# Performance work log

Hardware: AMD Instinct MI355X
Metric: run time of the kernel (lower is better)

The kernel has to match this reference:

```python
import jax, jax.numpy as jnp
import numpy as np

B, T, U = 2048, 200, 128


def setup_inputs() -> dict:
    key = jax.random.key(0)
    ks = jax.random.split(key, 9)
    s = 1.0 / np.sqrt(U)
    inp = {
        "interest_states": jax.random.normal(ks[0], (B, T, U), dtype=jnp.float32),
        "attention_scores": jax.random.uniform(ks[1], (B, T, 1), dtype=jnp.float32),
        "W_xu": jax.random.normal(ks[2], (U, U), dtype=jnp.float32) * s,
        "b_xu": jnp.zeros((U,), dtype=jnp.float32),
        "W_hu": jax.random.normal(ks[3], (U, U), dtype=jnp.float32) * s,
        "b_hu": jnp.zeros((U,), dtype=jnp.float32),
        "W_xr": jax.random.normal(ks[4], (U, U), dtype=jnp.float32) * s,
        "b_xr": jnp.zeros((U,), dtype=jnp.float32),
        "W_hr": jax.random.normal(ks[5], (U, U), dtype=jnp.float32) * s,
        "b_hr": jnp.zeros((U,), dtype=jnp.float32),
        "W_xc": jax.random.normal(ks[6], (U, U), dtype=jnp.float32) * s,
        "b_xc": jnp.zeros((U,), dtype=jnp.float32),
        "W_hc": jax.random.normal(ks[7], (U, U), dtype=jnp.float32) * s,
        "b_hc": jnp.zeros((U,), dtype=jnp.float32),
    }
    return inp


def reference(interest_states, attention_scores, W_xu, b_xu, W_hu, b_hu,
              W_xr, b_xr, W_hr, b_hr, W_xc, b_xc, W_hc, b_hc):
    # Precompute input-side projections for all timesteps (batched GEMMs).
    xu = jnp.einsum('btu,uv->btv', interest_states, W_xu) + b_xu  # [B,T,U]
    xr = jnp.einsum('btu,uv->btv', interest_states, W_xr) + b_xr
    xc = jnp.einsum('btu,uv->btv', interest_states, W_xc) + b_xc
    # Time-major for scan: [T,B,U] / [T,B,1]
    xu_t = jnp.swapaxes(xu, 0, 1)
    xr_t = jnp.swapaxes(xr, 0, 1)
    xc_t = jnp.swapaxes(xc, 0, 1)
    att_t = jnp.swapaxes(attention_scores, 0, 1)  # [T,B,1]

    def step(h, inp):
        xu_i, xr_i, xc_i, a_i = inp
        u = jax.nn.sigmoid(xu_i + h @ W_hu + b_hu)       # update gate [B,U]
        r = jax.nn.sigmoid(xr_i + h @ W_hr + b_hr)       # reset gate  [B,U]
        c = jnp.tanh(xc_i + (r * h) @ W_hc + b_hc)       # candidate   [B,U]
        au = a_i * u                                     # attention-scaled update gate
        h_new = (1.0 - au) * h + au * c
        return h_new, None

    h0 = jnp.zeros((interest_states.shape[0], W_hu.shape[0]), dtype=interest_states.dtype)
    h_final, _ = jax.lax.scan(step, h0, (xu_t, xr_t, xc_t, att_t))
    return h_final  # [B,U]
```

## Files before the change

### kernel.cpp

```cpp
#include <hip/hip_runtime.h>
#include <hip/hip_bf16.h>

#define B_  2048
#define T_  200
#define U_  128
#define NB  8
#define PITCH 136

typedef __attribute__((ext_vector_type(8))) short short8;
typedef __attribute__((ext_vector_type(2))) short short2_t;
typedef __attribute__((ext_vector_type(4))) float f32x4;
typedef __attribute__((ext_vector_type(2))) float f32x2;

static __device__ inline short f2bf(float f) {
  union { float f; unsigned u; } v; v.f = f;
  unsigned r = v.u + 0x7FFFu + ((v.u >> 16) & 1u);
  return (short)(r >> 16);
}
static __device__ inline float sigm(float x) {
  return __builtin_amdgcn_rcpf(1.0f + __builtin_amdgcn_exp2f(x * -1.44269504088896340736f));
}
static __device__ inline float tanh_fast(float x) {
  return 1.0f - 2.0f * __builtin_amdgcn_rcpf(1.0f + __builtin_amdgcn_exp2f(x * 2.88539008177792681472f));
}

__global__ void prep_weights(const float* __restrict__ Wxu, const float* __restrict__ Wxr,
                             const float* __restrict__ Wxc, const float* __restrict__ Whu,
                             const float* __restrict__ Whr, const float* __restrict__ Whc,
                             short* __restrict__ out) {
  const int m = blockIdx.x >> 7;
  const int k = blockIdx.x & 127;
  const int n = threadIdx.x;
  const float* Wp;
  switch (m) {
    case 0: Wp = Wxu; break; case 1: Wp = Wxr; break; case 2: Wp = Wxc; break;
    case 3: Wp = Whu; break; case 4: Wp = Whr; break; default: Wp = Whc; break;
  }
  out[(m * 128 + n) * 128 + k] = f2bf(Wp[k * 128 + n]);
}

__global__ __launch_bounds__(512, 2) void augru_scan(
    const float* __restrict__ IS, const float* __restrict__ ATT,
    const float* __restrict__ bxu, const float* __restrict__ bhu,
    const float* __restrict__ bxr, const float* __restrict__ bhr,
    const float* __restrict__ bxc, const float* __restrict__ bhc,
    const short* __restrict__ WT, float* __restrict__ out) {
  __shared__ short h_bf[16][PITCH];
  __shared__ short x_bf[16][PITCH];
  __shared__ short rh_bf[16][PITCH];
  __shared__ float att_s[T_][NB];

  const int tid  = threadIdx.x;
  const int w    = tid >> 6;
  const int l    = tid & 63;
  const int l15  = l & 15;
  const int lg   = l >> 4;
  const int b0   = blockIdx.x * NB;
  const int colb = w * 16;
  const int col  = colb + l15;

  for (int i = tid; i < 16 * PITCH / 2; i += 512) {
    ((int*)h_bf)[i] = 0; ((int*)x_bf)[i] = 0; ((int*)rh_bf)[i] = 0;
  }
  for (int i = tid; i < T_ * NB; i += 512) {
    int r = i / T_, t = i % T_;
    att_s[t][r] = ATT[(size_t)(b0 + r) * T_ + t];
  }
  const int prow = w;
  const int pc2  = (tid & 63) * 2;
  {
    f32x2 xv = *(const f32x2*)(IS + ((size_t)(b0 + prow) * T_ + 0) * U_ + pc2);
    short2_t xb; xb[0] = f2bf(xv[0]); xb[1] = f2bf(xv[1]);
    *(short2_t*)&x_bf[prow][pc2] = xb;
  }
  short8 Wf[6][4];
#pragma unroll
  for (int m = 0; m < 6; ++m)
#pragma unroll
    for (int kf = 0; kf < 4; ++kf)
      Wf[m][kf] = *(const short8*)(WT + ((m * 128 + col) * 128 + kf * 32 + lg * 8));
  const float bu = bxu[col] + bhu[col];
  const float br = bxr[col] + bhr[col];
  const float bc = bxc[col] + bhc[col];

  const f32x4 fz = {0.0f, 0.0f, 0.0f, 0.0f};
  f32x4 hreg = fz;
  float ureg[4];

  for (int t = 0; t < T_; ++t) {
    __syncthreads();
    short8 xa[4], ha[4];
#pragma unroll
    for (int kf = 0; kf < 4; ++kf) {
      xa[kf] = *(const short8*)&x_bf[l15][kf * 32 + lg * 8];
      ha[kf] = *(const short8*)&h_bf[l15][kf * 32 + lg * 8];
    }
    const int tn = (t < T_ - 1) ? t + 1 : t;
    f32x2 xnext = *(const f32x2*)(IS + ((size_t)(b0 + prow) * T_ + tn) * U_ + pc2);

    f32x4 axu = fz, axr = fz, axc = fz, ahu = fz, ahr = fz;
#pragma unroll
    for (int kf = 0; kf < 4; ++kf) {
      axu = __builtin_amdgcn_mfma_f32_16x16x32_bf16(xa[kf], Wf[0][kf], axu, 0, 0, 0);
      axr = __builtin_amdgcn_mfma_f32_16x16x32_bf16(xa[kf], Wf[1][kf], axr, 0, 0, 0);
      axc = __builtin_amdgcn_mfma_f32_16x16x32_bf16(xa[kf], Wf[2][kf], axc, 0, 0, 0);
      ahu = __builtin_amdgcn_mfma_f32_16x16x32_bf16(ha[kf], Wf[3][kf], ahu, 0, 0, 0);
      ahr = __builtin_amdgcn_mfma_f32_16x16x32_bf16(ha[kf], Wf[4][kf], ahr, 0, 0, 0);
    }
#pragma unroll
    for (int rg = 0; rg < 4; ++rg) {
      float ug = sigm(axu[rg] + ahu[rg] + bu);
      float rr = sigm(axr[rg] + ahr[rg] + br);
      ureg[rg] = ug;
      rh_bf[lg * 4 + rg][col] = f2bf(rr * hreg[rg]);
    }
    __syncthreads();
    short8 ra[4];
#pragma unroll
    for (int kf = 0; kf < 4; ++kf) ra[kf] = *(const short8*)&rh_bf[l15][kf * 32 + lg * 8];
    f32x4 ahc = fz;
#pragma unroll
    for (int kf = 0; kf < 4; ++kf)
      ahc = __builtin_amdgcn_mfma_f32_16x16x32_bf16(ra[kf], Wf[5][kf], ahc, 0, 0, 0);
    f32x4 a4 = *(const f32x4*)&att_s[t][(lg & 1) * 4];
#pragma unroll
    for (int rg = 0; rg < 4; ++rg) {
      float cc = tanh_fast(axc[rg] + ahc[rg] + bc);
      float au = a4[rg] * ureg[rg];
      float hv = (1.0f - au) * hreg[rg] + au * cc;
      hreg[rg] = hv;
      h_bf[lg * 4 + rg][col] = f2bf(hv);
    }
    {
      short2_t xb; xb[0] = f2bf(xnext[0]); xb[1] = f2bf(xnext[1]);
      *(short2_t*)&x_bf[prow][pc2] = xb;
    }
  }
#pragma unroll
  for (int rg = 0; rg < 4; ++rg) {
    const int row = lg * 4 + rg;
    if (row < NB) out[(size_t)(b0 + row) * U_ + col] = hreg[rg];
  }
}

extern "C" void kernel_launch(void* const* d_in, const int* in_sizes, int n_in,
                              void* d_out, int out_size, void* d_ws, size_t ws_size,
                              hipStream_t stream) {
  const float* IS  = (const float*)d_in[0];
  const float* ATT = (const float*)d_in[1];
  const float* Wxu = (const float*)d_in[2];  const float* bxu = (const float*)d_in[3];
  const float* Whu = (const float*)d_in[4];  const float* bhu = (const float*)d_in[5];
  const float* Wxr = (const float*)d_in[6];  const float* bxr = (const float*)d_in[7];
  const float* Whr = (const float*)d_in[8];  const float* bhr = (const float*)d_in[9];
  const float* Wxc = (const float*)d_in[10]; const float* bxc = (const float*)d_in[11];
  const float* Whc = (const float*)d_in[12]; const float* bhc = (const float*)d_in[13];
  short* WT  = (short*)d_ws;
  float* OUT = (float*)d_out;

  prep_weights<<<dim3(6 * 128), dim3(128), 0, stream>>>(Wxu, Wxr, Wxc, Whu, Whr, Whc, WT);
  augru_scan<<<dim3(B_ / NB), dim3(512), 0, stream>>>(IS, ATT, bxu, bhu, bxr, bhr, bxc, bhc, WT, OUT);
}
```

Baseline: 450.9 us.

## Store recurrent state transposed and load MFMA fragments with ds_read_b64_tr_b16

The h and r*h shared buffers now use a column-major [128][16] layout. Each lane writes one packed 64-bit word instead of four scattered bf16 stores, and the A fragments are read back with the gfx950 transposing LDS load ds_read_b64_tr_b16. Bias scaling is folded into the exp2 argument, bf16 packing uses the hardware pair conversion, the candidate MFMA chain is split into two accumulators to shorten the dependency, and explicit waitcnt and sched barriers fix the instruction order. The inline asm and hard-coded offsets depend on the exact LDS layout and on gfx950 support, and the manual scheduling barriers may block compiler interleaving.

New measurement: 449.2 us. About the same (-0.4%).

```diff
diff --git a/kernel.cpp b/kernel.cpp
--- a/kernel.cpp
+++ b/kernel.cpp
@@ -8,21 +8,43 @@
 #define PITCH 136
 
 typedef __attribute__((ext_vector_type(8))) short short8;
-typedef __attribute__((ext_vector_type(2))) short short2_t;
 typedef __attribute__((ext_vector_type(4))) float f32x4;
 typedef __attribute__((ext_vector_type(2))) float f32x2;
-
+typedef __attribute__((ext_vector_type(2))) unsigned uint2v;
+
+static __device__ inline float sigm_pre(float sum, float bS) {
+  float e = __builtin_amdgcn_exp2f(fmaf(sum, -1.44269504088896340736f, bS));
+  return __builtin_amdgcn_rcpf(1.0f + e);
+}
+static __device__ inline float tanh_pre(float sum, float bS) {
+  float e = __builtin_amdgcn_exp2f(fmaf(sum, 2.88539008177792681472f, bS));
+  float r = __builtin_amdgcn_rcpf(1.0f + e);
+  return fmaf(-2.0f, r, 1.0f);
+}
+static __device__ inline unsigned pk2(float a, float b) {
+  union { __hip_bfloat162 h; unsigned u; } c;
+  float2 t; t.x = a; t.y = b;
+  c.h = __float22bfloat162_rn(t);
+  return c.u;
+}
 static __device__ inline short f2bf(float f) {
   union { float f; unsigned u; } v; v.f = f;
   unsigned r = v.u + 0x7FFFu + ((v.u >> 16) & 1u);
   return (short)(r >> 16);
 }
-static __device__ inline float sigm(float x) {
-  return __builtin_amdgcn_rcpf(1.0f + __builtin_amdgcn_exp2f(x * -1.44269504088896340736f));
-}
-static __device__ inline float tanh_fast(float x) {
-  return 1.0f - 2.0f * __builtin_amdgcn_rcpf(1.0f + __builtin_amdgcn_exp2f(x * 2.88539008177792681472f));
-}
+
+#define TRFRAG(dst, addr, O0, O1)                                              \
+  {                                                                            \
+    uint2v _ta, _tb;                                                           \
+    asm volatile("ds_read_b64_tr_b16 %0, %1 offset:" O0 : "=v"(_ta) : "v"(addr)); \
+    asm volatile("ds_read_b64_tr_b16 %0, %1 offset:" O1 : "=v"(_tb) : "v"(addr)); \
+    union { struct { uint2v a, b; } p; short8 s; } _u;                         \
+    _u.p.a = _ta; _u.p.b = _tb;                                                \
+    dst = _u.s;                                                                \
+  }
+#define LGKM_WAIT()                                                            \
+  asm volatile("s_waitcnt lgkmcnt(0)" ::: "memory");                           \
+  __builtin_amdgcn_sched_barrier(0)
 
 __global__ void prep_weights(const float* __restrict__ Wxu, const float* __restrict__ Wxr,
                              const float* __restrict__ Wxc, const float* __restrict__ Whu,
@@ -45,10 +67,10 @@
     const float* __restrict__ bxr, const float* __restrict__ bhr,
     const float* __restrict__ bxc, const float* __restrict__ bhc,
     const short* __restrict__ WT, float* __restrict__ out) {
-  __shared__ short h_bf[16][PITCH];
-  __shared__ short x_bf[16][PITCH];
-  __shared__ short rh_bf[16][PITCH];
-  __shared__ float att_s[T_][NB];
+  __shared__ __align__(128) short h_T[128][16];
+  __shared__ __align__(128) short rh_T[128][16];
+  __shared__ __align__(16)  short x_bf[16][PITCH];
+  __shared__ __align__(16)  float att_s[T_][NB];
 
   const int tid  = threadIdx.x;
   const int w    = tid >> 6;
@@ -56,11 +78,12 @@
   const int l15  = l & 15;
   const int lg   = l >> 4;
   const int b0   = blockIdx.x * NB;
-  const int colb = w * 16;
-  const int col  = colb + l15;
-
-  for (int i = tid; i < 16 * PITCH / 2; i += 512) {
-    ((int*)h_bf)[i] = 0; ((int*)x_bf)[i] = 0; ((int*)rh_bf)[i] = 0;
+  const int col  = w * 16 + l15;
+
+  for (int i = tid; i < (128 * 16 * 2 + 16 * PITCH) / 2; i += 512) {
+    if (i < 128 * 16 / 2)               ((int*)h_T)[i] = 0;
+    else if (i < 128 * 16)              ((int*)rh_T)[i - 128 * 16 / 2] = 0;
+    else                                ((int*)x_bf)[i - 128 * 16] = 0;
   }
   for (int i = tid; i < T_ * NB; i += 512) {
     int r = i / T_, t = i % T_;
@@ -68,10 +91,10 @@
   }
   const int prow = w;
   const int pc2  = (tid & 63) * 2;
+  const float* xptr = IS + (size_t)(b0 + prow) * T_ * U_ + pc2;
   {
-    f32x2 xv = *(const f32x2*)(IS + ((size_t)(b0 + prow) * T_ + 0) * U_ + pc2);
-    short2_t xb; xb[0] = f2bf(xv[0]); xb[1] = f2bf(xv[1]);
-    *(short2_t*)&x_bf[prow][pc2] = xb;
+    f32x2 xv = *(const f32x2*)xptr;
+    *(unsigned*)&x_bf[prow][pc2] = pk2(xv[0], xv[1]);
   }
   short8 Wf[6][4];
 #pragma unroll
@@ -79,9 +102,18 @@
 #pragma unroll
     for (int kf = 0; kf < 4; ++kf)
       Wf[m][kf] = *(const short8*)(WT + ((m * 128 + col) * 128 + kf * 32 + lg * 8));
-  const float bu = bxu[col] + bhu[col];
-  const float br = bxr[col] + bhr[col];
-  const float bc = bxc[col] + bhc[col];
+#pragma unroll
+  for (int m = 0; m < 6; ++m)
+#pragma unroll
+    for (int kf = 0; kf < 4; ++kf) asm volatile("" : "+v"(Wf[m][kf]));
+
+  const float buS = (bxu[col] + bhu[col]) * -1.44269504088896340736f;
+  const float brS = (bxr[col] + bhr[col]) * -1.44269504088896340736f;
+  const float bcS = (bxc[col] + bhc[col]) * 2.88539008177792681472f;
+
+  const unsigned trv   = (unsigned)(lg * 256 + l15 * 8);
+  const unsigned adr_h = (unsigned)(size_t)(&h_T[0][0]) + trv;
+  const unsigned adr_r = (unsigned)(size_t)(&rh_T[0][0]) + trv;
 
   const f32x4 fz = {0.0f, 0.0f, 0.0f, 0.0f};
   f32x4 hreg = fz;
@@ -89,14 +121,17 @@
 
   for (int t = 0; t < T_; ++t) {
     __syncthreads();
-    short8 xa[4], ha[4];
-#pragma unroll
-    for (int kf = 0; kf < 4; ++kf) {
+    __builtin_amdgcn_sched_barrier(0);
+    short8 ha[4], xa[4];
+    TRFRAG(ha[0], adr_h, "0",    "128");
+    TRFRAG(ha[1], adr_h, "1024", "1152");
+    TRFRAG(ha[2], adr_h, "2048", "2176");
+    TRFRAG(ha[3], adr_h, "3072", "3200");
+#pragma unroll
+    for (int kf = 0; kf < 4; ++kf)
       xa[kf] = *(const short8*)&x_bf[l15][kf * 32 + lg * 8];
-      ha[kf] = *(const short8*)&h_bf[l15][kf * 32 + lg * 8];
-    }
-    const int tn = (t < T_ - 1) ? t + 1 : t;
-    f32x2 xnext = *(const f32x2*)(IS + ((size_t)(b0 + prow) * T_ + tn) * U_ + pc2);
+    const f32x2 xnext = *(const f32x2*)(xptr + (t < T_ - 1 ? (size_t)(t + 1) * U_ : (size_t)t * U_));
+    LGKM_WAIT();
 
     f32x4 axu = fz, axr = fz, axc = fz, ahu = fz, ahr = fz;
 #pragma unroll
@@ -107,34 +142,46 @@
       ahu = __builtin_amdgcn_mfma_f32_16x16x32_bf16(ha[kf], Wf[3][kf], ahu, 0, 0, 0);
       ahr = __builtin_amdgcn_mfma_f32_16x16x32_bf16(ha[kf], Wf[4][kf], ahr, 0, 0, 0);
     }
+    float rh[4];
 #pragma unroll
     for (int rg = 0; rg < 4; ++rg) {
-      float ug = sigm(axu[rg] + ahu[rg] + bu);
-      float rr = sigm(axr[rg] + ahr[rg] + br);
-      ureg[rg] = ug;
-      rh_bf[lg * 4 + rg][col] = f2bf(rr * hreg[rg]);
+      ureg[rg] = sigm_pre(axu[rg] + ahu[rg], buS);
+      float rr = sigm_pre(axr[rg] + ahr[rg], brS);
+      rh[rg]   = rr * hreg[rg];
+    }
+    {
+      uint2v wv; wv[0] = pk2(rh[0], rh[1]); wv[1] = pk2(rh[2], rh[3]);
+      *(uint2v*)&rh_T[col][lg * 4] = wv;
     }
     __syncthreads();
+    __builtin_amdgcn_sched_barrier(0);
     short8 ra[4];
-#pragma unroll
-    for (int kf = 0; kf < 4; ++kf) ra[kf] = *(const short8*)&rh_bf[l15][kf * 32 + lg * 8];
-    f32x4 ahc = fz;
-#pragma unroll
-    for (int kf = 0; kf < 4; ++kf)
-      ahc = __builtin_amdgcn_mfma_f32_16x16x32_bf16(ra[kf], Wf[5][kf], ahc, 0, 0, 0);
-    f32x4 a4 = *(const f32x4*)&att_s[t][(lg & 1) * 4];
+    TRFRAG(ra[0], adr_r, "0",    "128");
+    TRFRAG(ra[1], adr_r, "1024", "1152");
+    TRFRAG(ra[2], adr_r, "2048", "2176");
+    TRFRAG(ra[3], adr_r, "3072", "3200");
+    const f32x4 a4 = *(const f32x4*)&att_s[t][(lg & 1) * 4];
+    LGKM_WAIT();
+
+    f32x4 ahc0 = fz, ahc1 = fz;
+    ahc0 = __builtin_amdgcn_mfma_f32_16x16x32_bf16(ra[0], Wf[5][0], ahc0, 0, 0, 0);
+    ahc1 = __builtin_amdgcn_mfma_f32_16x16x32_bf16(ra[2], Wf[5][2], ahc1, 0, 0, 0);
+    ahc0 = __builtin_amdgcn_mfma_f32_16x16x32_bf16(ra[1], Wf[5][1], ahc0, 0, 0, 0);
+    ahc1 = __builtin_amdgcn_mfma_f32_16x16x32_bf16(ra[3], Wf[5][3], ahc1, 0, 0, 0);
+
+    float hv[4];
 #pragma unroll
     for (int rg = 0; rg < 4; ++rg) {
-      float cc = tanh_fast(axc[rg] + ahc[rg] + bc);
+      float cc = tanh_pre((axc[rg] + ahc0[rg]) + ahc1[rg], bcS);
       float au = a4[rg] * ureg[rg];
-      float hv = (1.0f - au) * hreg[rg] + au * cc;
-      hreg[rg] = hv;
-      h_bf[lg * 4 + rg][col] = f2bf(hv);
+      hv[rg] = fmaf(au, cc - hreg[rg], hreg[rg]);
+      hreg[rg] = hv[rg];
     }
     {
-      short2_t xb; xb[0] = f2bf(xnext[0]); xb[1] = f2bf(xnext[1]);
-      *(short2_t*)&x_bf[prow][pc2] = xb;
-    }
+      uint2v wv; wv[0] = pk2(hv[0], hv[1]); wv[1] = pk2(hv[2], hv[3]);
+      *(uint2v*)&h_T[col][lg * 4] = wv;
+    }
+    *(unsigned*)&x_bf[prow][pc2] = pk2(xnext[0], xnext[1]);
   }
 #pragma unroll
   for (int rg = 0; rg < 4; ++rg) {
```
